# Kernel tuning notes

Measured on AMD Instinct MI355X. Metric: run time of the kernel, lower is better.

The kernel has to match this reference:

```python
import jax, jax.numpy as jnp
import numpy as np

B, L, D_IN = 8, 512, 1024
HEAD_SIZE = 64
NUM_LABELS = 16
INF = 1e12


def _rotary_sin_cos(seq_len, dim):
    # HF RoFormerSinusoidalPositionalEmbedding: inv_freq = 10000^(-2i/dim)
    pos = np.arange(seq_len, dtype=np.float64)[:, None]
    inv_freq = 1.0 / np.power(10000.0, 2.0 * np.arange(dim // 2) / dim)
    ang = pos * inv_freq  # [L, dim//2]
    # interleave: [s0, s0, s1, s1, ...] (matches stack([sin,sin],-1).reshape)
    sin = jnp.asarray(np.repeat(np.sin(ang), 2, axis=-1), dtype=jnp.float32)
    cos = jnp.asarray(np.repeat(np.cos(ang), 2, axis=-1), dtype=jnp.float32)
    return sin[None], cos[None]  # [1, L, dim]


def _rotate_half(x):
    # [-x1, x0, -x3, x2, ...]
    return jnp.stack([-x[..., 1::2], x[..., ::2]], axis=-1).reshape(x.shape)


def setup_inputs() -> dict:
    key = jax.random.key(0)
    k1, k2, k3, k4, k5 = jax.random.split(key, 5)
    s1 = 1.0 / np.sqrt(D_IN)
    s2 = 1.0 / np.sqrt(2 * HEAD_SIZE)
    return {
        "inputs": jax.random.normal(k1, (B, L, D_IN), dtype=jnp.float32),
        "attention_mask": jnp.ones((B, L), dtype=jnp.int32),
        "W1": jax.random.uniform(k2, (D_IN, 2 * HEAD_SIZE), jnp.float32, -s1, s1),
        "b1": jax.random.uniform(k3, (2 * HEAD_SIZE,), jnp.float32, -s1, s1),
        "W2": jax.random.uniform(k4, (2 * HEAD_SIZE, 2 * NUM_LABELS), jnp.float32, -s2, s2),
        "b2": jax.random.uniform(k5, (2 * NUM_LABELS,), jnp.float32, -s2, s2),
    }


def reference(inputs, attention_mask, W1, b1, W2, b2):
    h = inputs @ W1 + b1                      # [B, L, 2*head_size]
    qw, kw = h[..., ::2], h[..., 1::2]        # [B, L, head_size]

    sin, cos = _rotary_sin_cos(h.shape[1], HEAD_SIZE)
    qw = qw * cos + _rotate_half(qw) * sin
    kw = kw * cos + _rotate_half(kw) * sin

    logits = jnp.einsum("bmd,bnd->bmn", qw, kw) / (HEAD_SIZE ** 0.5)  # [B, L, L]

    bias = (h @ W2 + b2).transpose(0, 2, 1) / 2.0        # [B, 2*heads, L]
    logits = logits[:, None] + bias[:, ::2, None, :] + bias[:, 1::2, :, None]  # [B, heads, L, L]

    am = attention_mask.astype(logits.dtype)
    attn_mask = 1.0 - am[:, None, None, :] * am[:, None, :, None]
    logits = logits - attn_mask * INF

    tril = jnp.tril(jnp.ones((h.shape[1], h.shape[1]), logits.dtype), k=-1)
    logits = logits - tril * INF
    return logits
```

## Files before the change

kernel.cpp:

```cpp
#include <hip/hip_runtime.h>
#include <math.h>

#define B_   8
#define L_   512
#define DIN  1024
#define H_   128
#define HEAD 64
#define NL   16
#define INF_ 1.0e12f

#define SIN_OFF  0
#define COS_OFF  (512*32)
#define QROT_OFF (COS_OFF + 512*32)
#define KROT_OFF (QROT_OFF + B_*L_*HEAD)
#define BQ_OFF   (KROT_OFF + B_*L_*HEAD)
#define BK_OFF   (BQ_OFF + B_*NL*L_)
#define QK_OFF   (BK_OFF + B_*NL*L_)
#define W1T_OFF  (QK_OFF + B_*L_*L_)
#define W2T_OFF  (W1T_OFF + 65536)

typedef float          floatx4  __attribute__((ext_vector_type(4)));
typedef short          shortx8  __attribute__((ext_vector_type(8)));
typedef unsigned short ushortx8 __attribute__((ext_vector_type(8)));

__device__ __forceinline__ unsigned short f2bf(float f) {
    unsigned u = __float_as_uint(f);
    u += 0x7FFFu + ((u >> 16) & 1u);
    return (unsigned short)(u >> 16);
}

__global__ __launch_bounds__(256) void prep_kernel(const float* __restrict__ W1,
                                                   const float* __restrict__ W2,
                                                   float* __restrict__ ws) {
    __shared__ float lds[64 * 132];
    const int tid = threadIdx.x;
    const int bid = blockIdx.x;

    if (bid < 64) {
        int idx = bid * 256 + tid;
        int m = idx >> 5, i = idx & 31;
        double ang = (double)m * pow(10000.0, -(double)i / 32.0);
        ws[SIN_OFF + idx] = (float)sin(ang);
        ws[COS_OFF + idx] = (float)cos(ang);
    } else if (bid < 80) {
        const int k0 = (bid - 64) * 64;
        for (int i = 0; i < 8; i++) {
            int f = tid + i * 256;
            int k = f >> 5, n4 = (f & 31) * 4;
            *(float4*)&lds[k * 132 + n4] = *(const float4*)&W1[(size_t)(k0 + k) * H_ + n4];
        }
        __syncthreads();
        unsigned short* W1T = (unsigned short*)(ws + W1T_OFF);
        const int n  = tid >> 1;
        const int kh = (tid & 1) * 32;
        for (int i = 0; i < 4; i++) {
            ushortx8 p;
            #pragma unroll
            for (int j = 0; j < 8; j++) p[j] = f2bf(lds[(kh + i * 8 + j) * 132 + n]);
            *(ushortx8*)&W1T[(size_t)n * DIN + k0 + kh + i * 8] = p;
        }
    } else {
        unsigned short* W2T = (unsigned short*)(ws + W2T_OFF);
        const int o  = tid >> 3;
        const int kc = (tid & 7) * 16;
        ushortx8 p0, p1;
        #pragma unroll
        for (int j = 0; j < 8; j++) p0[j] = f2bf(W2[(size_t)(kc + j) * 32 + o]);
        #pragma unroll
        for (int j = 0; j < 8; j++) p1[j] = f2bf(W2[(size_t)(kc + 8 + j) * 32 + o]);
        *(ushortx8*)&W2T[(size_t)o * H_ + kc]     = p0;
        *(ushortx8*)&W2T[(size_t)o * H_ + kc + 8] = p1;
    }
}

__global__ __launch_bounds__(256) void gemm1_fused_kernel(
    const float* __restrict__ X, const float* __restrict__ b1,
    const float* __restrict__ b2, float* __restrict__ ws)
{
    __shared__ float hs[16 * 132];

    const int tid  = threadIdx.x;
    const int m0   = blockIdx.x * 16;
    const int w    = tid >> 6;
    const int lane = tid & 63;
    const int lrow = lane >> 4;
    const int lcol = lane & 15;

    const unsigned short* W1T = (const unsigned short*)(ws + W1T_OFF);

    const float* pA = X + (size_t)(m0 + lcol) * DIN + lrow * 8;
    const unsigned short* pB0 = W1T + (size_t)(w * 32 + lcol) * DIN + lrow * 8;
    const unsigned short* pB1 = pB0 + (size_t)16 * DIN;

    floatx4 acc0 = {0.f, 0.f, 0.f, 0.f};
    floatx4 acc1 = {0.f, 0.f, 0.f, 0.f};

    #pragma unroll
    for (int s = 0; s < 32; s++) {
        float4 a0 = *(const float4*)(pA + s * 32);
        float4 a1 = *(const float4*)(pA + s * 32 + 4);
        shortx8 bf0 = *(const shortx8*)(pB0 + s * 32);
        shortx8 bf1 = *(const shortx8*)(pB1 + s * 32);
        ushortx8 afu;
        afu[0] = f2bf(a0.x); afu[1] = f2bf(a0.y); afu[2] = f2bf(a0.z); afu[3] = f2bf(a0.w);
        afu[4] = f2bf(a1.x); afu[5] = f2bf(a1.y); afu[6] = f2bf(a1.z); afu[7] = f2bf(a1.w);
        shortx8 af = (shortx8)afu;
        acc0 = __builtin_amdgcn_mfma_f32_16x16x32_bf16(af, bf0, acc0, 0, 0, 0);
        acc1 = __builtin_amdgcn_mfma_f32_16x16x32_bf16(af, bf1, acc1, 0, 0, 0);
    }

    {
        float b1a = b1[w * 32 + lcol];
        float b1b = b1[w * 32 + 16 + lcol];
        #pragma unroll
        for (int r = 0; r < 4; r++) {
            hs[(lrow * 4 + r) * 132 + w * 32 + lcol]      = acc0[r] + b1a;
            hs[(lrow * 4 + r) * 132 + w * 32 + 16 + lcol] = acc1[r] + b1b;
        }
    }
    __syncthreads();

    {
        int row = tid >> 4;
        int j   = tid & 15;
        int g   = m0 + row;
        int pos = g & (L_ - 1);
        const float* hr = &hs[row * 132];
        float h0 = hr[8 * j + 0], h1 = hr[8 * j + 1];
        float h2 = hr[8 * j + 2], h3 = hr[8 * j + 3];
        float h4 = hr[8 * j + 4], h5 = hr[8 * j + 5];
        float h6 = hr[8 * j + 6], h7 = hr[8 * j + 7];
        float s0 = ws[SIN_OFF + pos * 32 + 2 * j];
        float c0 = ws[COS_OFF + pos * 32 + 2 * j];
        float s1 = ws[SIN_OFF + pos * 32 + 2 * j + 1];
        float c1 = ws[COS_OFF + pos * 32 + 2 * j + 1];
        float4 q, k;
        q.x = h0 * c0 - h2 * s0;  q.y = h2 * c0 + h0 * s0;
        q.z = h4 * c1 - h6 * s1;  q.w = h6 * c1 + h4 * s1;
        k.x = h1 * c0 - h3 * s0;  k.y = h3 * c0 + h1 * s0;
        k.z = h5 * c1 - h7 * s1;  k.w = h7 * c1 + h5 * s1;
        *(float4*)&ws[QROT_OFF + (size_t)g * HEAD + 4 * j] = q;
        *(float4*)&ws[KROT_OFF + (size_t)g * HEAD + 4 * j] = k;
    }

    if (w == 0) {
        const unsigned short* W2T = (const unsigned short*)(ws + W2T_OFF);
        floatx4 bacc0 = {0.f, 0.f, 0.f, 0.f};
        floatx4 bacc1 = {0.f, 0.f, 0.f, 0.f};
        #pragma unroll
        for (int s = 0; s < 4; s++) {
            int k = s * 32 + lrow * 8;
            ushortx8 hfu;
            #pragma unroll
            for (int j = 0; j < 8; j++) hfu[j] = f2bf(hs[lcol * 132 + k + j]);
            shortx8 hf = (shortx8)hfu;
            shortx8 wf0 = *(const shortx8*)(W2T + (size_t)lcol * H_ + k);
            shortx8 wf1 = *(const shortx8*)(W2T + (size_t)(16 + lcol) * H_ + k);
            bacc0 = __builtin_amdgcn_mfma_f32_16x16x32_bf16(hf, wf0, bacc0, 0, 0, 0);
            bacc1 = __builtin_amdgcn_mfma_f32_16x16x32_bf16(hf, wf1, bacc1, 0, 0, 0);
        }
        float b2a = b2[lcol], b2b = b2[16 + lcol];
        #pragma unroll
        for (int r = 0; r < 4; r++) {
            int g   = m0 + lrow * 4 + r;
            int bb  = g >> 9;
            int pos = g & (L_ - 1);
            float v0 = (bacc0[r] + b2a) * 0.5f;
            float v1 = (bacc1[r] + b2b) * 0.5f;
            int o0 = lcol, o1 = 16 + lcol;
            if (o0 & 1) ws[BQ_OFF + ((size_t)bb * NL + (o0 >> 1)) * L_ + pos] = v0;
            else        ws[BK_OFF + ((size_t)bb * NL + (o0 >> 1)) * L_ + pos] = v0;
            if (o1 & 1) ws[BQ_OFF + ((size_t)bb * NL + (o1 >> 1)) * L_ + pos] = v1;
            else        ws[BK_OFF + ((size_t)bb * NL + (o1 >> 1)) * L_ + pos] = v1;
        }
    }
}

__global__ __launch_bounds__(256) void qk_kernel(float* __restrict__ ws)
{
    __shared__ float Qs[64][68];
    __shared__ float Ks[64][68];

    const int tid = threadIdx.x;
    const int bid = blockIdx.x;
    const int bb = bid >> 6;
    const int mt = (bid >> 3) & 7;
    const int nt = bid & 7;
    const int m0 = mt * 64, n0 = nt * 64;

    {
        int r0   = tid >> 4;
        int dcol = (tid & 15) * 4;
        #pragma unroll
        for (int rr = 0; rr < 4; rr++) {
            int r = r0 + rr * 16;
            float4 q = *(const float4*)&ws[QROT_OFF + ((size_t)(bb * L_ + m0 + r)) * HEAD + dcol];
            float4 k = *(const float4*)&ws[KROT_OFF + ((size_t)(bb * L_ + n0 + r)) * HEAD + dcol];
            Qs[dcol + 0][r] = q.x; Qs[dcol + 1][r] = q.y;
            Qs[dcol + 2][r] = q.z; Qs[dcol + 3][r] = q.w;
            Ks[dcol + 0][r] = k.x; Ks[dcol + 1][r] = k.y;
            Ks[dcol + 2][r] = k.z; Ks[dcol + 3][r] = k.w;
        }
    }
    __syncthreads();

    const int ty = tid >> 4;
    const int tx = tid & 15;
    float acc[4][4] = {};
    #pragma unroll 8
    for (int d = 0; d < HEAD; d++) {
        float4 a  = *(const float4*)&Qs[d][ty * 4];
        float4 bv = *(const float4*)&Ks[d][tx * 4];
        acc[0][0] += a.x * bv.x; acc[0][1] += a.x * bv.y; acc[0][2] += a.x * bv.z; acc[0][3] += a.x * bv.w;
        acc[1][0] += a.y * bv.x; acc[1][1] += a.y * bv.y; acc[1][2] += a.y * bv.z; acc[1][3] += a.y * bv.w;
        acc[2][0] += a.z * bv.x; acc[2][1] += a.z * bv.y; acc[2][2] += a.z * bv.z; acc[2][3] += a.z * bv.w;
        acc[3][0] += a.w * bv.x; acc[3][1] += a.w * bv.y; acc[3][2] += a.w * bv.z; acc[3][3] += a.w * bv.w;
    }

    #pragma unroll
    for (int r = 0; r < 4; r++) {
        float4 o;
        o.x = acc[r][0] * 0.125f; o.y = acc[r][1] * 0.125f;
        o.z = acc[r][2] * 0.125f; o.w = acc[r][3] * 0.125f;
        *(float4*)&ws[QK_OFF + ((size_t)(bb * L_ + m0 + ty * 4 + r)) * L_ + n0 + tx * 4] = o;
    }
}

__global__ __launch_bounds__(128) void bcast_kernel(
    const int* __restrict__ am, const float* __restrict__ ws, float* __restrict__ out)
{
    const int bm = blockIdx.x;
    const int bb = bm >> 9;
    const int m  = bm & (L_ - 1);
    const int n0 = threadIdx.x * 4;

    float4 qk4 = *(const float4*)&ws[QK_OFF + ((size_t)(bb * L_ + m)) * L_ + n0];
    float amm = (float)am[bb * L_ + m];
    int4 amn = *(const int4*)&am[bb * L_ + n0];

    float4 base;
    base.x = qk4.x - (1.0f - amm * (float)amn.x) * INF_ - ((n0 + 0 < m) ? INF_ : 0.0f);
    base.y = qk4.y - (1.0f - amm * (float)amn.y) * INF_ - ((n0 + 1 < m) ? INF_ : 0.0f);
    base.z = qk4.z - (1.0f - amm * (float)amn.z) * INF_ - ((n0 + 2 < m) ? INF_ : 0.0f);
    base.w = qk4.w - (1.0f - amm * (float)amn.w) * INF_ - ((n0 + 3 < m) ? INF_ : 0.0f);

    #pragma unroll
    for (int l = 0; l < NL; l++) {
        float  bq  = ws[BQ_OFF + ((size_t)bb * NL + l) * L_ + m];
        float4 bk4 = *(const float4*)&ws[BK_OFF + ((size_t)bb * NL + l) * L_ + n0];
        float4 o;
        o.x = base.x + bk4.x + bq;
        o.y = base.y + bk4.y + bq;
        o.z = base.z + bk4.z + bq;
        o.w = base.w + bk4.w + bq;
        *(float4*)&out[(((size_t)(bb * NL + l)) * L_ + m) * L_ + n0] = o;
    }
}

extern "C" void kernel_launch(void* const* d_in, const int* in_sizes, int n_in,
                              void* d_out, int out_size, void* d_ws, size_t ws_size,
                              hipStream_t stream) {
    const float* X  = (const float*)d_in[0];
    const int*   am = (const int*)d_in[1];
    const float* W1 = (const float*)d_in[2];
    const float* b1 = (const float*)d_in[3];
    const float* W2 = (const float*)d_in[4];
    const float* b2 = (const float*)d_in[5];
    float* out = (float*)d_out;
    float* ws  = (float*)d_ws;

    prep_kernel<<<81, 256, 0, stream>>>(W1, W2, ws);
    gemm1_fused_kernel<<<(B_ * L_) / 16, 256, 0, stream>>>(X, b1, b2, ws);
    qk_kernel<<<B_ * (L_ / 64) * (L_ / 64), 256, 0, stream>>>(ws);
    bcast_kernel<<<B_ * L_, 128, 0, stream>>>(am, ws, out);
}
```

Before: 60.36 us.

## Fuse QK matmul with mask and label-bias broadcast into one kernel

Merges the QK tile kernel and the broadcast kernel so each 64x64 logits tile is computed in registers, masked, and written directly for all 16 labels. This removes the intermediate B*L*L QK buffer round-trip through global memory and one kernel launch. Bias rows and mask values are staged in LDS per block. The output write pattern changes from full-row float4 stores to 4-row tile stores of 256 bytes per row segment, and only 512 blocks now carry the large output write.

```diff
diff --git a/kernel.cpp b/kernel.cpp
--- a/kernel.cpp
+++ b/kernel.cpp
@@ -15,8 +15,7 @@
 #define KROT_OFF (QROT_OFF + B_*L_*HEAD)
 #define BQ_OFF   (KROT_OFF + B_*L_*HEAD)
 #define BK_OFF   (BQ_OFF + B_*NL*L_)
-#define QK_OFF   (BK_OFF + B_*NL*L_)
-#define W1T_OFF  (QK_OFF + B_*L_*L_)
+#define W1T_OFF  (BK_OFF + B_*NL*L_)
 #define W2T_OFF  (W1T_OFF + 65536)
 
 typedef float          floatx4  __attribute__((ext_vector_type(4)));
@@ -176,10 +175,15 @@
     }
 }
 
-__global__ __launch_bounds__(256) void qk_kernel(float* __restrict__ ws)
+__global__ __launch_bounds__(256) void qk_bcast_kernel(
+    const int* __restrict__ am, const float* __restrict__ ws, float* __restrict__ out)
 {
     __shared__ float Qs[64][68];
     __shared__ float Ks[64][68];
+    __shared__ float BQs[16][64];
+    __shared__ float BKs[16][64];
+    __shared__ float maskM[64];
+    __shared__ float maskN[64];
 
     const int tid = threadIdx.x;
     const int bid = blockIdx.x;
@@ -202,6 +206,14 @@
             Ks[dcol + 2][r] = k.z; Ks[dcol + 3][r] = k.w;
         }
     }
+    {
+        int l = tid >> 4;
+        int c = (tid & 15) * 4;
+        *(float4*)&BQs[l][c] = *(const float4*)&ws[BQ_OFF + ((size_t)bb * NL + l) * L_ + m0 + c];
+        *(float4*)&BKs[l][c] = *(const float4*)&ws[BK_OFF + ((size_t)bb * NL + l) * L_ + n0 + c];
+    }
+    if (tid < 64)       maskM[tid]      = (float)am[bb * L_ + m0 + tid];
+    else if (tid < 128) maskN[tid - 64] = (float)am[bb * L_ + n0 + (tid - 64)];
     __syncthreads();
 
     const int ty = tid >> 4;
@@ -217,43 +229,35 @@
         acc[3][0] += a.w * bv.x; acc[3][1] += a.w * bv.y; acc[3][2] += a.w * bv.z; acc[3][3] += a.w * bv.w;
     }
 
+    float4 base[4];
     #pragma unroll
     for (int r = 0; r < 4; r++) {
-        float4 o;
-        o.x = acc[r][0] * 0.125f; o.y = acc[r][1] * 0.125f;
-        o.z = acc[r][2] * 0.125f; o.w = acc[r][3] * 0.125f;
-        *(float4*)&ws[QK_OFF + ((size_t)(bb * L_ + m0 + ty * 4 + r)) * L_ + n0 + tx * 4] = o;
-    }
-}
-
-__global__ __launch_bounds__(128) void bcast_kernel(
-    const int* __restrict__ am, const float* __restrict__ ws, float* __restrict__ out)
-{
-    const int bm = blockIdx.x;
-    const int bb = bm >> 9;
-    const int m  = bm & (L_ - 1);
-    const int n0 = threadIdx.x * 4;
-
-    float4 qk4 = *(const float4*)&ws[QK_OFF + ((size_t)(bb * L_ + m)) * L_ + n0];
-    float amm = (float)am[bb * L_ + m];
-    int4 amn = *(const int4*)&am[bb * L_ + n0];
-
-    float4 base;
-    base.x = qk4.x - (1.0f - amm * (float)amn.x) * INF_ - ((n0 + 0 < m) ? INF_ : 0.0f);
-    base.y = qk4.y - (1.0f - amm * (float)amn.y) * INF_ - ((n0 + 1 < m) ? INF_ : 0.0f);
-    base.z = qk4.z - (1.0f - amm * (float)amn.z) * INF_ - ((n0 + 2 < m) ? INF_ : 0.0f);
-    base.w = qk4.w - (1.0f - amm * (float)amn.w) * INF_ - ((n0 + 3 < m) ? INF_ : 0.0f);
+        int m = m0 + ty * 4 + r;
+        float mm = maskM[ty * 4 + r];
+        #pragma unroll
+        for (int c = 0; c < 4; c++) {
+            int n = n0 + tx * 4 + c;
+            float v = acc[r][c] * 0.125f
+                    - (1.0f - mm * maskN[tx * 4 + c]) * INF_
+                    - ((n < m) ? INF_ : 0.0f);
+            ((float*)&base[r])[c] = v;
+        }
+    }
 
     #pragma unroll
     for (int l = 0; l < NL; l++) {
-        float  bq  = ws[BQ_OFF + ((size_t)bb * NL + l) * L_ + m];
-        float4 bk4 = *(const float4*)&ws[BK_OFF + ((size_t)bb * NL + l) * L_ + n0];
-        float4 o;
-        o.x = base.x + bk4.x + bq;
-        o.y = base.y + bk4.y + bq;
-        o.z = base.z + bk4.z + bq;
-        o.w = base.w + bk4.w + bq;
-        *(float4*)&out[(((size_t)(bb * NL + l)) * L_ + m) * L_ + n0] = o;
+        float4 bk4 = *(const float4*)&BKs[l][tx * 4];
+        size_t outb = (((size_t)(bb * NL + l)) * L_ + m0 + ty * 4) * L_ + n0 + tx * 4;
+        #pragma unroll
+        for (int r = 0; r < 4; r++) {
+            float bq = BQs[l][ty * 4 + r];
+            float4 o;
+            o.x = base[r].x + bk4.x + bq;
+            o.y = base[r].y + bk4.y + bq;
+            o.z = base[r].z + bk4.z + bq;
+            o.w = base[r].w + bk4.w + bq;
+            *(float4*)&out[outb + (size_t)r * L_] = o;
+        }
     }
 }
 
@@ -271,6 +275,5 @@
 
     prep_kernel<<<81, 256, 0, stream>>>(W1, W2, ws);
     gemm1_fused_kernel<<<(B_ * L_) / 16, 256, 0, stream>>>(X, b1, b2, ws);
-    qk_kernel<<<B_ * (L_ / 64) * (L_ / 64), 256, 0, stream>>>(ws);
-    bcast_kernel<<<B_ * L_, 128, 0, stream>>>(am, ws, out);
-}
+    qk_bcast_kernel<<<B_ * (L_ / 64) * (L_ / 64), 256, 0, stream>>>(am, ws, out);
+}
```

After: 53.91 us. 10.7% less time.
